# Performance work log

Measured on AMD Instinct MI355X. Metric: run time of the kernel, lower is better.

## Reference

```python
import jax, jax.numpy as jnp
import numpy as np

B, S, D, H, FF = 2, 2048, 1024, 16, 4096
HD = D // H          # head dim = 64
ROT = HD // 2        # rotary dim = dim/(num_heads*2) = 32 (partial rotation)
EPS = 1e-5


def setup_inputs() -> dict:
    key = jax.random.key(0)
    ks = jax.random.split(key, 16)
    std = 0.02
    return {
        "x": jax.random.normal(ks[0], (B, S, D), jnp.float32),
        "mask": jnp.ones((B, 1, 1, S), jnp.int32),
        "wq": jax.random.normal(ks[1], (D, D), jnp.float32) * std,
        "bq": jnp.zeros((D,), jnp.float32),
        "wk": jax.random.normal(ks[2], (D, D), jnp.float32) * std,
        "bk": jnp.zeros((D,), jnp.float32),
        "wv": jax.random.normal(ks[3], (D, D), jnp.float32) * std,
        "bv": jnp.zeros((D,), jnp.float32),
        "wo": jax.random.normal(ks[4], (D, D), jnp.float32) * std,
        "bo": jnp.zeros((D,), jnp.float32),
        "ln1_w": jnp.ones((D,), jnp.float32),
        "ln1_b": jnp.zeros((D,), jnp.float32),
        "ln2_w": jnp.ones((D,), jnp.float32),
        "ln2_b": jnp.zeros((D,), jnp.float32),
        "w1": jax.random.normal(ks[5], (D, FF), jnp.float32) * std,
        "b1": jnp.zeros((FF,), jnp.float32),
        "w2": jax.random.normal(ks[6], (FF, D), jnp.float32) * std,
        "b2": jnp.zeros((D,), jnp.float32),
    }


def _layernorm(x, w, b):
    mu = jnp.mean(x, axis=-1, keepdims=True)
    var = jnp.mean(jnp.square(x - mu), axis=-1, keepdims=True)
    return (x - mu) * jax.lax.rsqrt(var + EPS) * w + b


def _rope(t):
    # t: [B, H, S, HD]; rotate first ROT features, interleaved (GPT-J) pairing
    inv_freq = 1.0 / (10000.0 ** (jnp.arange(0, ROT, 2, dtype=jnp.float32) / ROT))
    ang = jnp.arange(S, dtype=jnp.float32)[:, None] * inv_freq      # [S, ROT//2]
    ang = jnp.repeat(ang, 2, axis=-1)                               # [S, ROT]
    cos, sin = jnp.cos(ang), jnp.sin(ang)
    t_rot, t_pass = t[..., :ROT], t[..., ROT:]
    pr = t_rot.reshape(*t_rot.shape[:-1], ROT // 2, 2)
    rot = jnp.stack([-pr[..., 1], pr[..., 0]], axis=-1).reshape(t_rot.shape)
    return jnp.concatenate([t_rot * cos + rot * sin, t_pass], axis=-1)


def reference(x, mask, wq, bq, wk, bk, wv, bv, wo, bo,
              ln1_w, ln1_b, ln2_w, ln2_b, w1, b1, w2, b2):
    res = x
    h = _layernorm(x, ln1_w, ln1_b)
    q = (h @ wq + bq).reshape(B, S, H, HD).transpose(0, 2, 1, 3)
    k = (h @ wk + bk).reshape(B, S, H, HD).transpose(0, 2, 1, 3)
    v = (h @ wv + bv).reshape(B, S, H, HD).transpose(0, 2, 1, 3)
    q, k = _rope(q), _rope(k)
    score = jnp.einsum('bhqd,bhkd->bhqk', q, k) * (1.0 / np.sqrt(HD))
    score = jnp.where(mask == 0, jnp.float32(-1e9), score)
    attn = jax.nn.softmax(score, axis=-1)
    out = jnp.einsum('bhqk,bhkd->bhqd', attn, v)
    out = out.transpose(0, 2, 1, 3).reshape(B, S, D) @ wo + bo
    x = res + out
    res = x
    h = _layernorm(x, ln2_w, ln2_b)
    h = jax.nn.gelu(h @ w1 + b1, approximate=False) @ w2 + b2
    return res + h
```

## Files before the change

### kernel.cpp

```cpp
#include <hip/hip_runtime.h>
#include <cstdint>
#include <cstddef>


typedef __bf16 bf16;
typedef __bf16 bf16x2 __attribute__((ext_vector_type(2)));
typedef __bf16 bf16x4v __attribute__((ext_vector_type(4)));
typedef __bf16 bf16x8 __attribute__((ext_vector_type(8)));
typedef float  f32x4  __attribute__((ext_vector_type(4)));

#define NB 2
#define NS 2048
#define ND 1024
#define NH 16
#define NHD 64
#define NFF 4096
#define NM (NB*NS)
#define QKSCALE 0.18033688011112042f

typedef uint32_t __attribute__((address_space(1))) gu32_t;
typedef uint32_t __attribute__((address_space(3))) lu32_t;
__device__ __forceinline__ void async_copy16(void* lds, const void* g) {
  __builtin_amdgcn_global_load_lds((gu32_t*)g, (lu32_t*)lds, 16, 0, 0);
}

__device__ __forceinline__ bf16x4v tr_read16(const void* p) {
  typedef const __attribute__((address_space(3))) unsigned char* lp;
  bf16x4v d;
  asm volatile("ds_read_b64_tr_b16 %0, %1" : "=v"(d) : "v"((lp)p));
  return d;
}

__device__ __forceinline__ float gelu_f(float x) {
  return 0.5f * x * (1.0f + erff(x * 0.70710678118654752f));
}

__global__ __launch_bounds__(256) void transpose_all(
    const float* __restrict__ wq, const float* __restrict__ wk,
    const float* __restrict__ wv, const float* __restrict__ wo,
    const float* __restrict__ w1, const float* __restrict__ w2,
    bf16* __restrict__ wqt, bf16* __restrict__ wkt, bf16* __restrict__ wvt,
    bf16* __restrict__ wot, bf16* __restrict__ w1t, bf16* __restrict__ w2t) {
  __shared__ float t[32][33];
  int flat = blockIdx.x;
  const float* W; bf16* Wt; long bx, by; int K, N;
  if (flat < 4096) {
    int which = flat >> 10, r = flat & 1023;
    const float* Ws[4] = {wq, wk, wv, wo};
    bf16* Wts[4] = {wqt, wkt, wvt, wot};
    W = Ws[which]; Wt = Wts[which]; bx = r & 31; by = r >> 5; K = ND; N = ND;
  } else if (flat < 8192) {
    int r = flat - 4096;
    W = w1; Wt = w1t; bx = r & 127; by = r >> 7; K = ND; N = NFF;
  } else {
    int r = flat - 8192;
    W = w2; Wt = w2t; bx = r & 31; by = r >> 5; K = NFF; N = ND;
  }
  int tx = threadIdx.x, ty = threadIdx.y;
#pragma unroll
  for (int r = 0; r < 4; ++r)
    t[ty + r*8][tx] = W[(by*32 + ty + r*8) * (long)N + bx*32 + tx];
  __syncthreads();
#pragma unroll
  for (int r = 0; r < 4; ++r)
    Wt[(bx*32 + ty + r*8) * (long)K + by*32 + tx] = (bf16)t[tx][ty + r*8];
}

__global__ __launch_bounds__(256) void smallfuse_kernel(
    const float* __restrict__ a, const float* __restrict__ b,
    const float* __restrict__ c, float* __restrict__ o,
    const int* __restrict__ mask, float* __restrict__ mb) {
  int blk = blockIdx.x;
  int t = threadIdx.x;
  if (blk < 12) {
    int i = blk * 256 + t;
    o[i] = (i < ND) ? a[i] : ((i < 2*ND) ? b[i - ND] : c[i - 2*ND]);
  } else {
    int i = (blk - 12) * 256 + t;
    mb[i] = mask[i] ? 0.0f : -1.0e9f;
  }
}

__global__ __launch_bounds__(256) void ln_kernel(
    const float* __restrict__ x, const float* __restrict__ w,
    const float* __restrict__ b, bf16* __restrict__ out) {
  long row = blockIdx.x;
  int t = threadIdx.x;
  float4 v = ((const float4*)(x + row*ND))[t];
  float s  = v.x + v.y + v.z + v.w;
  float sq = v.x*v.x + v.y*v.y + v.z*v.z + v.w*v.w;
#pragma unroll
  for (int m = 1; m <= 32; m <<= 1) { s += __shfl_xor(s, m); sq += __shfl_xor(sq, m); }
  __shared__ float ss[4], ssq[4];
  if ((t & 63) == 0) { ss[t>>6] = s; ssq[t>>6] = sq; }
  __syncthreads();
  s  = ss[0] + ss[1] + ss[2] + ss[3];
  sq = ssq[0] + ssq[1] + ssq[2] + ssq[3];
  float mu = s * (1.0f/ND);
  float rs = rsqrtf(sq * (1.0f/ND) - mu*mu + 1e-5f);
  float4 wv = ((const float4*)w)[t];
  float4 bv = ((const float4*)b)[t];
  bf16x4v o;
  o[0] = (bf16)((v.x-mu)*rs*wv.x + bv.x);
  o[1] = (bf16)((v.y-mu)*rs*wv.y + bv.y);
  o[2] = (bf16)((v.z-mu)*rs*wv.z + bv.z);
  o[3] = (bf16)((v.w-mu)*rs*wv.w + bv.w);
  *(bf16x4v*)(out + row*ND + t*4) = o;
}

__global__ __launch_bounds__(256) void rope_kernel(bf16* __restrict__ q,
                                                   bf16* __restrict__ k) {
  long tid = (long)blockIdx.x * 256 + threadIdx.x;
  int i = (int)(tid & 15);
  int h = (int)((tid >> 4) & 15);
  long bs = tid >> 8;
  int s = (int)(bs & (NS - 1));
  float ang = (float)s * exp2f(-(float)i * (13.287712379549449f / 16.0f));
  float sn, cs;
  sincosf(ang, &sn, &cs);
  long base = bs * ND + h * NHD + 2*i;
  bf16x2* qp = (bf16x2*)(q + base);
  bf16x2 qv = *qp;
  float q0 = (float)qv[0], q1 = (float)qv[1];
  bf16x2 qo; qo[0] = (bf16)(q0*cs - q1*sn); qo[1] = (bf16)(q1*cs + q0*sn);
  *qp = qo;
  bf16x2* kp = (bf16x2*)(k + base);
  bf16x2 kv = *kp;
  float k0 = (float)kv[0], k1 = (float)kv[1];
  bf16x2 ko; ko[0] = (bf16)(k0*cs - k1*sn); ko[1] = (bf16)(k1*cs + k0*sn);
  *kp = ko;
}

template<int EPI>
__global__ __launch_bounds__(256) void gemm_kernel(
    const bf16* __restrict__ A, const bf16* __restrict__ Bt,
    const float* __restrict__ bias, const float* __restrict__ res,
    void* __restrict__ Cout, int M, int N, int K) {
  __shared__ __align__(16) bf16 Alds[2][128*32];
  __shared__ __align__(16) bf16 Blds[2][128*32];
  const int tid = threadIdx.x, lane = tid & 63, w = tid >> 6;
  const int fr = lane & 15, k8 = (lane >> 4) * 8;
  const int wm = (w >> 1) * 64, wn = (w & 1) * 64;

  const int gx = gridDim.x;
  int lin = blockIdx.y * gx + blockIdx.x;
  int nwg = gx * gridDim.y;
  int swz = (lin & 7) * (nwg >> 3) + (lin >> 3);
  const long am0 = (long)(swz / gx) * 128;
  const long bn0 = (long)(swz % gx) * 128;

  const f32x4 fzero = {0.f, 0.f, 0.f, 0.f};
  f32x4 acc[4][4];
#pragma unroll
  for (int m = 0; m < 4; ++m)
#pragma unroll
    for (int n = 0; n < 4; ++n) acc[m][n] = fzero;

  auto stage = [&](int kt, int bufi) {
#pragma unroll
    for (int i = 0; i < 2; ++i) {
      int slot = i*256 + tid;
      int r = slot >> 2, c = slot & 3;
      async_copy16((char*)&Alds[bufi][0] + i*4096 + w*1024,
                   &A[(am0 + r)*K + kt + c*8]);
      async_copy16((char*)&Blds[bufi][0] + i*4096 + w*1024,
                   &Bt[(bn0 + r)*K + kt + c*8]);
    }
  };

  const int nk = K >> 5;
  stage(0, 0);
  asm volatile("s_waitcnt vmcnt(0)" ::: "memory");
  __builtin_amdgcn_s_barrier();
  __builtin_amdgcn_sched_barrier(0);

  for (int t = 0; t < nk; ++t) {
    const int cur = t & 1;
    if (t + 1 < nk) stage((t + 1) * 32, cur ^ 1);
    const bf16* Ab = &Alds[cur][0];
    const bf16* Bb = &Blds[cur][0];
    bf16x8 af[4], bfv[4];
#pragma unroll
    for (int m = 0; m < 4; ++m) af[m]  = *(const bf16x8*)&Ab[(wm + m*16 + fr)*32 + k8];
#pragma unroll
    for (int n = 0; n < 4; ++n) bfv[n] = *(const bf16x8*)&Bb[(wn + n*16 + fr)*32 + k8];
#pragma unroll
    for (int m = 0; m < 4; ++m)
#pragma unroll
      for (int n = 0; n < 4; ++n)
        acc[m][n] = __builtin_amdgcn_mfma_f32_16x16x32_bf16(af[m], bfv[n], acc[m][n], 0, 0, 0);
    asm volatile("s_waitcnt vmcnt(0)" ::: "memory");
    __builtin_amdgcn_s_barrier();
    __builtin_amdgcn_sched_barrier(0);
  }

  const int rbase = (lane >> 4) * 4;
#pragma unroll
  for (int m = 0; m < 4; ++m) {
#pragma unroll
    for (int n = 0; n < 4; ++n) {
      long col = bn0 + wn + n*16 + fr;
      float bia = bias[col];
#pragma unroll
      for (int j = 0; j < 4; ++j) {
        long row = am0 + wm + m*16 + rbase + j;
        float val = acc[m][n][j] + bia;
        if (EPI == 1) {
          ((bf16*)Cout)[row * N + col] = (bf16)gelu_f(val);
        } else if (EPI == 2) {
          ((float*)Cout)[row * N + col] = val + res[row * N + col];
        } else {
          long sub = col >> 10;
          float sv = (sub == 0) ? val * QKSCALE : val;
          ((bf16*)Cout)[sub * (long)(NM*(long)ND) + row * ND + (col & 1023)] = (bf16)sv;
        }
      }
    }
  }
}

template<int EPI>
__global__ __launch_bounds__(512, 2) void gemm256_kernel(
    const bf16* __restrict__ A, const bf16* __restrict__ Bt,
    const float* __restrict__ bias,
    void* __restrict__ Cout, int M, int N, int K) {
  __shared__ __align__(16) bf16 Alds[2][256*32];
  __shared__ __align__(16) bf16 Blds[2][256*32];
  const int tid = threadIdx.x, lane = tid & 63, w = tid >> 6;
  const int fr = lane & 15, k8 = (lane >> 4) * 8;
  const int wr = w >> 2, wc = w & 3;

  const int gx = gridDim.x;
  int lin = blockIdx.y * gx + blockIdx.x;
  int nwg = gx * gridDim.y;
  int swz = (lin & 7) * (nwg >> 3) + (lin >> 3);
  const long am0 = (long)(swz / gx) * 256;
  const long bn0 = (long)(swz % gx) * 256;

  const f32x4 fzero = {0.f, 0.f, 0.f, 0.f};
  f32x4 acc[8][4];
#pragma unroll
  for (int m = 0; m < 8; ++m)
#pragma unroll
    for (int n = 0; n < 4; ++n) acc[m][n] = fzero;

  auto stage = [&](int kt, int bufi) {
#pragma unroll
    for (int i = 0; i < 2; ++i) {
      int chunk = i*512 + tid;
      int r = chunk >> 2, c = chunk & 3;
      async_copy16((char*)&Alds[bufi][0] + i*8192 + w*1024,
                   &A[(am0 + r)*K + kt + c*8]);
      async_copy16((char*)&Blds[bufi][0] + i*8192 + w*1024,
                   &Bt[(bn0 + r)*K + kt + c*8]);
    }
  };

  const int nk = K >> 5;
  stage(0, 0);
  asm volatile("s_waitcnt vmcnt(0)" ::: "memory");
  __builtin_amdgcn_s_barrier();
  __builtin_amdgcn_sched_barrier(0);

  for (int t = 0; t < nk; ++t) {
    const int cur = t & 1;
    if (t + 1 < nk) stage((t + 1) * 32, cur ^ 1);
    const bf16* Ab = &Alds[cur][0];
    const bf16* Bb = &Blds[cur][0];
    bf16x8 af[4], bfv[4];
#pragma unroll
    for (int n = 0; n < 4; ++n) bfv[n] = *(const bf16x8*)&Bb[(wc*64 + n*16 + fr)*32 + k8];
#pragma unroll
    for (int m = 0; m < 4; ++m) af[m]  = *(const bf16x8*)&Ab[(wr*128 + m*16 + fr)*32 + k8];
    asm volatile("s_waitcnt lgkmcnt(0)" ::: "memory");
    __builtin_amdgcn_sched_barrier(0);
    __builtin_amdgcn_s_setprio(1);
#pragma unroll
    for (int m = 0; m < 4; ++m)
#pragma unroll
      for (int n = 0; n < 4; ++n)
        acc[m][n] = __builtin_amdgcn_mfma_f32_16x16x32_bf16(af[m], bfv[n], acc[m][n], 0, 0, 0);
    __builtin_amdgcn_s_setprio(0);
    __builtin_amdgcn_s_barrier();
#pragma unroll
    for (int m = 0; m < 4; ++m) af[m] = *(const bf16x8*)&Ab[(wr*128 + (m+4)*16 + fr)*32 + k8];
    asm volatile("s_waitcnt lgkmcnt(0)" ::: "memory");
    __builtin_amdgcn_sched_barrier(0);
    __builtin_amdgcn_s_setprio(1);
#pragma unroll
    for (int m = 0; m < 4; ++m)
#pragma unroll
      for (int n = 0; n < 4; ++n)
        acc[m+4][n] = __builtin_amdgcn_mfma_f32_16x16x32_bf16(af[m], bfv[n], acc[m+4][n], 0, 0, 0);
    __builtin_amdgcn_s_setprio(0);
    asm volatile("s_waitcnt vmcnt(0)" ::: "memory");
    __builtin_amdgcn_s_barrier();
    __builtin_amdgcn_sched_barrier(0);
  }

  const int rbase = (lane >> 4) * 4;
#pragma unroll
  for (int m = 0; m < 8; ++m) {
#pragma unroll
    for (int n = 0; n < 4; ++n) {
      long col = bn0 + wc*64 + n*16 + fr;
      float bia = bias[col];
#pragma unroll
      for (int j = 0; j < 4; ++j) {
        long row = am0 + wr*128 + m*16 + rbase + j;
        float val = acc[m][n][j] + bia;
        if (EPI == 1) {
          ((bf16*)Cout)[row * N + col] = (bf16)gelu_f(val);
        } else {
          long sub = col >> 10;
          float sv = (sub == 0) ? val * QKSCALE : val;
          ((bf16*)Cout)[sub * (long)(NM*(long)ND) + row * ND + (col & 1023)] = (bf16)sv;
        }
      }
    }
  }
}

__global__ __launch_bounds__(256) void attn_kernel(
    const bf16* __restrict__ q, const bf16* __restrict__ k,
    const bf16* __restrict__ v, const float* __restrict__ mbias,
    bf16* __restrict__ out) {
  int lin = blockIdx.y * 32 + blockIdx.x;
  int swz = (lin & 7) * 128 + (lin >> 3);
  const int qt = swz & 31;
  const int b = swz >> 9, h = (swz >> 5) & 15;
  const int tid = threadIdx.x, lane = tid & 63, w = tid >> 6;
  const int fr = lane & 15, kg = lane >> 4;
  const int k8 = kg * 8;
  const int frl = fr & 3, frh = fr >> 2;

  __shared__ __align__(16) bf16 Klds[2][64*64];
  __shared__ __align__(16) bf16 Vlds[2][64*64];

  const long qrow = (long)qt*64 + w*16 + fr;
  const bf16* qbase = q + ((long)b*NS + qrow)*ND + h*NHD;
  bf16x8 qf[2];
  qf[0] = *(const bf16x8*)(qbase + k8);
  qf[1] = *(const bf16x8*)(qbase + 32 + k8);

  const bf16* kbase = k + (long)b*NS*ND + h*NHD;
  const bf16* vbase = v + (long)b*NS*ND + h*NHD;

  auto stageK = [&](int kt, int bufi) {
#pragma unroll
    for (int i = 0; i < 2; ++i) {
      int slot = i*256 + tid;
      int row = slot >> 3, c = slot & 7;
      int csrc = c ^ (row & 7) ^ (((row >> 3) & 1) << 2);
      async_copy16((char*)&Klds[bufi][0] + i*4096 + w*1024,
                   kbase + ((long)kt*64 + row)*ND + csrc*8);
    }
  };
  auto stageV = [&](int kt, int bufi) {
#pragma unroll
    for (int i = 0; i < 2; ++i) {
      int kr = i*32 + (tid >> 5)*4 + ((tid & 7) >> 1);
      int dc = ((tid >> 3) & 3)*16 + (tid & 1)*8;
      async_copy16((char*)&Vlds[bufi][0] + i*4096 + w*1024,
                   vbase + ((long)kt*64 + kr)*ND + dc);
    }
  };

  const f32x4 fzero = {0.f, 0.f, 0.f, 0.f};
  f32x4 oacc[4];
#pragma unroll
  for (int n = 0; n < 4; ++n) oacc[n] = fzero;
  float lsum = 0.f;
  const float* mbb = mbias + (long)b*NS;

  stageK(0, 0);
  stageV(0, 0);
  asm volatile("s_waitcnt vmcnt(0)" ::: "memory");
  __builtin_amdgcn_s_barrier();
  __builtin_amdgcn_sched_barrier(0);

  const int NT = NS / 64;
  for (int kt = 0; kt < NT; ++kt) {
    const int cur = kt & 1;
    if (kt + 1 < NT) { stageK(kt + 1, cur ^ 1); stageV(kt + 1, cur ^ 1); }
    const char* Kb = (const char*)&Klds[cur][0];
    const char* Vb = (const char*)&Vlds[cur][0];

    f32x4 sacc[4];
#pragma unroll
    for (int n = 0; n < 4; ++n) sacc[n] = fzero;
#pragma unroll
    for (int n = 0; n < 4; ++n) {
      int r = (frh << 3) + ((n & 1) << 2) + frl + ((n >> 1) << 5);
      int swzr = (r & 7) ^ (((r >> 3) & 1) << 2);
#pragma unroll
      for (int kk = 0; kk < 2; ++kk) {
        bf16x8 kf = *(const bf16x8*)(Kb + r*128 + ((((kk << 2) | kg) ^ swzr) << 4));
        sacc[n] = __builtin_amdgcn_mfma_f32_16x16x32_bf16(kf, qf[kk], sacc[n], 0, 0, 0);
      }
    }

    float p[4][4];
#pragma unroll
    for (int n = 0; n < 4; ++n) {
      float4 mb = *(const float4*)&mbb[kt*64 + kg*8 + ((n & 1) << 2) + ((n >> 1) << 5)];
      p[n][0] = exp2f(sacc[n][0] + mb.x);
      p[n][1] = exp2f(sacc[n][1] + mb.y);
      p[n][2] = exp2f(sacc[n][2] + mb.z);
      p[n][3] = exp2f(sacc[n][3] + mb.w);
    }
#pragma unroll
    for (int n = 0; n < 4; ++n)
      lsum += (p[n][0] + p[n][1]) + (p[n][2] + p[n][3]);

    bf16x8 paf[2];
#pragma unroll
    for (int n = 0; n < 4; ++n) {
#pragma unroll
      for (int j = 0; j < 4; ++j)
        paf[n >> 1][((n & 1) << 2) + j] = (bf16)p[n][j];
    }

#pragma unroll
    for (int kk = 0; kk < 2; ++kk) {
      bf16x4v t0[4], t1[4];
#pragma unroll
      for (int n2 = 0; n2 < 4; ++n2) {
        t0[n2] = tr_read16(Vb + (((kk*8 + 0)*4 + n2)*128 + kg*1024 + fr*8));
        t1[n2] = tr_read16(Vb + (((kk*8 + 1)*4 + n2)*128 + kg*1024 + fr*8));
      }
      asm volatile("s_waitcnt lgkmcnt(0)" ::: "memory");
      __builtin_amdgcn_sched_barrier(0);
#pragma unroll
      for (int n2 = 0; n2 < 4; ++n2) {
        bf16x8 vb8 = __builtin_shufflevector(t0[n2], t1[n2], 0, 1, 2, 3, 4, 5, 6, 7);
        oacc[n2] = __builtin_amdgcn_mfma_f32_16x16x32_bf16(paf[kk], vb8, oacc[n2], 0, 0, 0);
      }
    }

    asm volatile("s_waitcnt vmcnt(0)" ::: "memory");
    __builtin_amdgcn_s_barrier();
    __builtin_amdgcn_sched_barrier(0);
  }

  lsum += __shfl_xor(lsum, 16);
  lsum += __shfl_xor(lsum, 32);
#pragma unroll
  for (int j = 0; j < 4; ++j) {
    float lj = __shfl(lsum, kg*4 + j);
    float inv = 1.0f / lj;
    long orow = (long)qt*64 + w*16 + kg*4 + j;
    bf16* ob = out + ((long)b*NS + orow)*ND + h*NHD;
#pragma unroll
    for (int n2 = 0; n2 < 4; ++n2) ob[n2*16 + fr] = (bf16)(oacc[n2][j] * inv);
  }
}

extern "C" void kernel_launch(void* const* d_in, const int* in_sizes, int n_in,
                              void* d_out, int out_size, void* d_ws, size_t ws_size,
                              hipStream_t stream) {
  const float* x    = (const float*)d_in[0];
  const int*   mask = (const int*)d_in[1];
  const float* wq   = (const float*)d_in[2];
  const float* bq   = (const float*)d_in[3];
  const float* wk   = (const float*)d_in[4];
  const float* bk   = (const float*)d_in[5];
  const float* wv   = (const float*)d_in[6];
  const float* bv   = (const float*)d_in[7];
  const float* wo   = (const float*)d_in[8];
  const float* bo   = (const float*)d_in[9];
  const float* ln1w = (const float*)d_in[10];
  const float* ln1b = (const float*)d_in[11];
  const float* ln2w = (const float*)d_in[12];
  const float* ln2b = (const float*)d_in[13];
  const float* w1   = (const float*)d_in[14];
  const float* b1   = (const float*)d_in[15];
  const float* w2   = (const float*)d_in[16];
  const float* b2   = (const float*)d_in[17];
  float* out = (float*)d_out;

  char* ws = (char*)d_ws;
  const size_t MB = 1024ull * 1024ull;
  bf16* wqt = (bf16*)(ws + 0*MB);
  bf16* wkt = (bf16*)(ws + 2*MB);
  bf16* wvt = (bf16*)(ws + 4*MB);
  bf16* wot = (bf16*)(ws + 6*MB);
  bf16* w1t = (bf16*)(ws + 8*MB);
  bf16* w2t = (bf16*)(ws + 16*MB);
  bf16* h1   = (bf16*)(ws + 24*MB);
  bf16* qb   = (bf16*)(ws + 32*MB);
  bf16* kb   = (bf16*)(ws + 40*MB);
  bf16* vb   = (bf16*)(ws + 48*MB);
  bf16* attn = h1;
  bf16* f1   = (bf16*)(ws + 24*MB);
  float* y1  = (float*)(ws + 56*MB);
  bf16* h2   = (bf16*)(ws + 72*MB);
  float* bcat = (float*)(ws + 80*MB);
  float* mbf  = (float*)(ws + 80*MB + 12*1024);
  (void)in_sizes; (void)n_in; (void)out_size; (void)ws_size;

  transpose_all<<<12288, dim3(32, 8), 0, stream>>>(wq, wk, wv, wo, w1, w2,
                                                   wqt, wkt, wvt, wot, w1t, w2t);
  smallfuse_kernel<<<28, 256, 0, stream>>>(bq, bk, bv, bcat, mask, mbf);

  ln_kernel<<<NM, 256, 0, stream>>>(x, ln1w, ln1b, h1);

  gemm256_kernel<3><<<dim3(12, 16), 512, 0, stream>>>(h1, wqt, bcat, qb,
                                                      NM, 3*ND, ND);
  rope_kernel<<<4096, 256, 0, stream>>>(qb, kb);
  attn_kernel<<<dim3(NS/64, NB*NH), 256, 0, stream>>>(qb, kb, vb, mbf, attn);

  gemm_kernel<2><<<dim3(8, 32), 256, 0, stream>>>(attn, wot, bo, x, y1,
                                                  NM, ND, ND);
  ln_kernel<<<NM, 256, 0, stream>>>(y1, ln2w, ln2b, h2);
  gemm256_kernel<1><<<dim3(16, 16), 512, 0, stream>>>(h2, w1t, b1, f1,
                                                      NM, NFF, ND);
  gemm_kernel<2><<<dim3(8, 32), 256, 0, stream>>>(f1, w2t, b2, y1, out,
                                                  NM, ND, NFF);
}
```

Before: 326.2 us.

## Deepen GEMM LDS pipeline, swizzle LDS layout, precompute RoPE table

Both GEMM kernels move from a 2-stage to a 4-buffer LDS ring that prefetches two K-tiles ahead, using partial vmcnt waits so loads overlap compute. LDS tiles are XOR-swizzled on the 16-byte chunk index to cut bank conflicts on fragment reads, and the 128-tile kernel gains explicit lgkmcnt waits, setprio and a launch bound of 2 blocks per CU. RoPE cos/sin values are now computed once per (s, i) into a table inside the small setup kernel rather than per element in the rope kernel. LDS use doubles, with 256-tile kernel at 128KB per block, which may limit occupancy.

```diff
diff --git a/kernel.cpp b/kernel.cpp
--- a/kernel.cpp
+++ b/kernel.cpp
@@ -69,15 +69,23 @@
 __global__ __launch_bounds__(256) void smallfuse_kernel(
     const float* __restrict__ a, const float* __restrict__ b,
     const float* __restrict__ c, float* __restrict__ o,
-    const int* __restrict__ mask, float* __restrict__ mb) {
+    const int* __restrict__ mask, float* __restrict__ mb,
+    float2* __restrict__ rtab) {
   int blk = blockIdx.x;
   int t = threadIdx.x;
   if (blk < 12) {
     int i = blk * 256 + t;
     o[i] = (i < ND) ? a[i] : ((i < 2*ND) ? b[i - ND] : c[i - 2*ND]);
-  } else {
+  } else if (blk < 28) {
     int i = (blk - 12) * 256 + t;
     mb[i] = mask[i] ? 0.0f : -1.0e9f;
+  } else {
+    int idx = (blk - 28) * 256 + t;
+    int s = idx >> 4, i = idx & 15;
+    float ang = (float)s * exp2f(-(float)i * (13.287712379549449f / 16.0f));
+    float sn, cs;
+    sincosf(ang, &sn, &cs);
+    rtab[idx] = make_float2(cs, sn);
   }
 }
 
@@ -109,15 +117,15 @@
 }
 
 __global__ __launch_bounds__(256) void rope_kernel(bf16* __restrict__ q,
-                                                   bf16* __restrict__ k) {
+                                                   bf16* __restrict__ k,
+                                                   const float2* __restrict__ rtab) {
   long tid = (long)blockIdx.x * 256 + threadIdx.x;
   int i = (int)(tid & 15);
   int h = (int)((tid >> 4) & 15);
   long bs = tid >> 8;
   int s = (int)(bs & (NS - 1));
-  float ang = (float)s * exp2f(-(float)i * (13.287712379549449f / 16.0f));
-  float sn, cs;
-  sincosf(ang, &sn, &cs);
+  float2 csn = rtab[(s << 4) | i];
+  float cs = csn.x, sn = csn.y;
   long base = bs * ND + h * NHD + 2*i;
   bf16x2* qp = (bf16x2*)(q + base);
   bf16x2 qv = *qp;
@@ -132,15 +140,16 @@
 }
 
 template<int EPI>
-__global__ __launch_bounds__(256) void gemm_kernel(
+__global__ __launch_bounds__(256, 2) void gemm_kernel(
     const bf16* __restrict__ A, const bf16* __restrict__ Bt,
     const float* __restrict__ bias, const float* __restrict__ res,
     void* __restrict__ Cout, int M, int N, int K) {
-  __shared__ __align__(16) bf16 Alds[2][128*32];
-  __shared__ __align__(16) bf16 Blds[2][128*32];
+  __shared__ __align__(16) bf16 Alds[4][128*32];
+  __shared__ __align__(16) bf16 Blds[4][128*32];
   const int tid = threadIdx.x, lane = tid & 63, w = tid >> 6;
-  const int fr = lane & 15, k8 = (lane >> 4) * 8;
+  const int fr = lane & 15, kg = lane >> 4;
   const int wm = (w >> 1) * 64, wn = (w & 1) * 64;
+  const int swb = (kg ^ ((fr >> 1) & 3)) << 4;
 
   const int gx = gridDim.x;
   int lin = blockIdx.y * gx + blockIdx.x;
@@ -159,8 +168,8 @@
   auto stage = [&](int kt, int bufi) {
 #pragma unroll
     for (int i = 0; i < 2; ++i) {
-      int slot = i*256 + tid;
-      int r = slot >> 2, c = slot & 3;
+      int s = i*256 + tid;
+      int r = s >> 2, c = (s & 3) ^ ((s >> 3) & 3);
       async_copy16((char*)&Alds[bufi][0] + i*4096 + w*1024,
                    &A[(am0 + r)*K + kt + c*8]);
       async_copy16((char*)&Blds[bufi][0] + i*4096 + w*1024,
@@ -170,31 +179,37 @@
 
   const int nk = K >> 5;
   stage(0, 0);
-  asm volatile("s_waitcnt vmcnt(0)" ::: "memory");
+  stage(32, 1);
+  asm volatile("s_waitcnt vmcnt(4)" ::: "memory");
   __builtin_amdgcn_s_barrier();
   __builtin_amdgcn_sched_barrier(0);
 
   for (int t = 0; t < nk; ++t) {
-    const int cur = t & 1;
-    if (t + 1 < nk) stage((t + 1) * 32, cur ^ 1);
-    const bf16* Ab = &Alds[cur][0];
-    const bf16* Bb = &Blds[cur][0];
+    const int cur = t & 3;
+    if (t + 2 < nk) stage((t + 2) * 32, (t + 2) & 3);
+    const char* Ab = (const char*)&Alds[cur][0];
+    const char* Bb = (const char*)&Blds[cur][0];
     bf16x8 af[4], bfv[4];
 #pragma unroll
-    for (int m = 0; m < 4; ++m) af[m]  = *(const bf16x8*)&Ab[(wm + m*16 + fr)*32 + k8];
-#pragma unroll
-    for (int n = 0; n < 4; ++n) bfv[n] = *(const bf16x8*)&Bb[(wn + n*16 + fr)*32 + k8];
+    for (int m = 0; m < 4; ++m) af[m]  = *(const bf16x8*)(Ab + (wm + m*16 + fr)*64 + swb);
+#pragma unroll
+    for (int n = 0; n < 4; ++n) bfv[n] = *(const bf16x8*)(Bb + (wn + n*16 + fr)*64 + swb);
+    asm volatile("s_waitcnt lgkmcnt(0)" ::: "memory");
+    __builtin_amdgcn_sched_barrier(0);
+    __builtin_amdgcn_s_setprio(1);
 #pragma unroll
     for (int m = 0; m < 4; ++m)
 #pragma unroll
       for (int n = 0; n < 4; ++n)
         acc[m][n] = __builtin_amdgcn_mfma_f32_16x16x32_bf16(af[m], bfv[n], acc[m][n], 0, 0, 0);
-    asm volatile("s_waitcnt vmcnt(0)" ::: "memory");
+    __builtin_amdgcn_s_setprio(0);
+    if (t + 2 < nk) { asm volatile("s_waitcnt vmcnt(4)" ::: "memory"); }
+    else            { asm volatile("s_waitcnt vmcnt(0)" ::: "memory"); }
     __builtin_amdgcn_s_barrier();
     __builtin_amdgcn_sched_barrier(0);
   }
 
-  const int rbase = (lane >> 4) * 4;
+  const int rbase = kg * 4;
 #pragma unroll
   for (int m = 0; m < 4; ++m) {
 #pragma unroll
@@ -224,11 +239,12 @@
     const bf16* __restrict__ A, const bf16* __restrict__ Bt,
     const float* __restrict__ bias,
     void* __restrict__ Cout, int M, int N, int K) {
-  __shared__ __align__(16) bf16 Alds[2][256*32];
-  __shared__ __align__(16) bf16 Blds[2][256*32];
+  __shared__ __align__(16) bf16 Alds[4][256*32];
+  __shared__ __align__(16) bf16 Blds[4][256*32];
   const int tid = threadIdx.x, lane = tid & 63, w = tid >> 6;
-  const int fr = lane & 15, k8 = (lane >> 4) * 8;
+  const int fr = lane & 15, kg = lane >> 4;
   const int wr = w >> 2, wc = w & 3;
+  const int swb = (kg ^ ((fr >> 1) & 3)) << 4;
 
   const int gx = gridDim.x;
   int lin = blockIdx.y * gx + blockIdx.x;
@@ -247,8 +263,8 @@
   auto stage = [&](int kt, int bufi) {
 #pragma unroll
     for (int i = 0; i < 2; ++i) {
-      int chunk = i*512 + tid;
-      int r = chunk >> 2, c = chunk & 3;
+      int s = i*512 + tid;
+      int r = s >> 2, c = (s & 3) ^ ((s >> 3) & 3);
       async_copy16((char*)&Alds[bufi][0] + i*8192 + w*1024,
                    &A[(am0 + r)*K + kt + c*8]);
       async_copy16((char*)&Blds[bufi][0] + i*8192 + w*1024,
@@ -258,20 +274,21 @@
 
   const int nk = K >> 5;
   stage(0, 0);
-  asm volatile("s_waitcnt vmcnt(0)" ::: "memory");
+  stage(32, 1);
+  asm volatile("s_waitcnt vmcnt(4)" ::: "memory");
   __builtin_amdgcn_s_barrier();
   __builtin_amdgcn_sched_barrier(0);
 
   for (int t = 0; t < nk; ++t) {
-    const int cur = t & 1;
-    if (t + 1 < nk) stage((t + 1) * 32, cur ^ 1);
-    const bf16* Ab = &Alds[cur][0];
-    const bf16* Bb = &Blds[cur][0];
+    const int cur = t & 3;
+    if (t + 2 < nk) stage((t + 2) * 32, (t + 2) & 3);
+    const char* Ab = (const char*)&Alds[cur][0];
+    const char* Bb = (const char*)&Blds[cur][0];
     bf16x8 af[4], bfv[4];
 #pragma unroll
-    for (int n = 0; n < 4; ++n) bfv[n] = *(const bf16x8*)&Bb[(wc*64 + n*16 + fr)*32 + k8];
-#pragma unroll
-    for (int m = 0; m < 4; ++m) af[m]  = *(const bf16x8*)&Ab[(wr*128 + m*16 + fr)*32 + k8];
+    for (int n = 0; n < 4; ++n) bfv[n] = *(const bf16x8*)(Bb + (wc*64 + n*16 + fr)*64 + swb);
+#pragma unroll
+    for (int m = 0; m < 4; ++m) af[m]  = *(const bf16x8*)(Ab + (wr*128 + m*16 + fr)*64 + swb);
     asm volatile("s_waitcnt lgkmcnt(0)" ::: "memory");
     __builtin_amdgcn_sched_barrier(0);
     __builtin_amdgcn_s_setprio(1);
@@ -283,7 +300,7 @@
     __builtin_amdgcn_s_setprio(0);
     __builtin_amdgcn_s_barrier();
 #pragma unroll
-    for (int m = 0; m < 4; ++m) af[m] = *(const bf16x8*)&Ab[(wr*128 + (m+4)*16 + fr)*32 + k8];
+    for (int m = 0; m < 4; ++m) af[m] = *(const bf16x8*)(Ab + (wr*128 + (m+4)*16 + fr)*64 + swb);
     asm volatile("s_waitcnt lgkmcnt(0)" ::: "memory");
     __builtin_amdgcn_sched_barrier(0);
     __builtin_amdgcn_s_setprio(1);
@@ -293,12 +310,13 @@
       for (int n = 0; n < 4; ++n)
         acc[m+4][n] = __builtin_amdgcn_mfma_f32_16x16x32_bf16(af[m], bfv[n], acc[m+4][n], 0, 0, 0);
     __builtin_amdgcn_s_setprio(0);
-    asm volatile("s_waitcnt vmcnt(0)" ::: "memory");
+    if (t + 2 < nk) { asm volatile("s_waitcnt vmcnt(4)" ::: "memory"); }
+    else            { asm volatile("s_waitcnt vmcnt(0)" ::: "memory"); }
     __builtin_amdgcn_s_barrier();
     __builtin_amdgcn_sched_barrier(0);
   }
 
-  const int rbase = (lane >> 4) * 4;
+  const int rbase = kg * 4;
 #pragma unroll
   for (int m = 0; m < 8; ++m) {
 #pragma unroll
@@ -496,18 +514,19 @@
   float* y1  = (float*)(ws + 56*MB);
   bf16* h2   = (bf16*)(ws + 72*MB);
   float* bcat = (float*)(ws + 80*MB);
-  float* mbf  = (float*)(ws + 80*MB + 12*1024);
+  float* mbf  = (float*)(ws + 80*MB + 16*1024);
+  float2* rtab = (float2*)(ws + 80*MB + 32*1024);
   (void)in_sizes; (void)n_in; (void)out_size; (void)ws_size;
 
   transpose_all<<<12288, dim3(32, 8), 0, stream>>>(wq, wk, wv, wo, w1, w2,
                                                    wqt, wkt, wvt, wot, w1t, w2t);
-  smallfuse_kernel<<<28, 256, 0, stream>>>(bq, bk, bv, bcat, mask, mbf);
+  smallfuse_kernel<<<156, 256, 0, stream>>>(bq, bk, bv, bcat, mask, mbf, rtab);
 
   ln_kernel<<<NM, 256, 0, stream>>>(x, ln1w, ln1b, h1);
 
   gemm256_kernel<3><<<dim3(12, 16), 512, 0, stream>>>(h1, wqt, bcat, qb,
                                                       NM, 3*ND, ND);
-  rope_kernel<<<4096, 256, 0, stream>>>(qb, kb);
+  rope_kernel<<<4096, 256, 0, stream>>>(qb, kb, rtab);
   attn_kernel<<<dim3(NS/64, NB*NH), 256, 0, stream>>>(qb, kb, vb, mbf, attn);
 
   gemm_kernel<2><<<dim3(8, 32), 256, 0, stream>>>(attn, wot, bo, x, y1,
```

New measurement: 328.9 us. About the same (+0.8%).
